# Optimization experiments

Hardware: AMD Instinct MI355X
Metric: run time of the kernel (lower is better)

The kernel has to match this reference:

```python
import jax, jax.numpy as jnp
import numpy as np
from jax import lax


def _lstm_encode(x_seq, W_ih, W_hh, b_ih, b_hh):
    """Run a single-layer LSTM over x_seq (B,S,F); return final (h, c), each (B,H).
    PyTorch gate order: i, f, g, o."""
    B = x_seq.shape[0]
    H = W_hh.shape[1]
    # Precompute input projections for the whole sequence: (B,S,4H)
    xg = jnp.einsum('bsf,gf->bsg', x_seq, W_ih) + b_ih + b_hh

    def step(carry, xg_t):
        h, c = carry
        gates = xg_t + h @ W_hh.T  # (B,4H)
        i, f, g, o = jnp.split(gates, 4, axis=-1)
        c = jax.nn.sigmoid(f) * c + jax.nn.sigmoid(i) * jnp.tanh(g)
        h = jax.nn.sigmoid(o) * jnp.tanh(c)
        return (h, c), None

    h0 = jnp.zeros((B, H), dtype=x_seq.dtype)
    c0 = jnp.zeros((B, H), dtype=x_seq.dtype)
    (h, c), _ = lax.scan(step, (h0, c0), jnp.swapaxes(xg, 0, 1))
    return h, c


def setup_inputs() -> dict:
    key = jax.random.key(0)
    ks = jax.random.split(key, 8)
    B, S, F, H, T = 256, 512, 64, 1024, 64
    s_in = 1.0 / np.sqrt(F)
    s_h = 1.0 / np.sqrt(H)
    return {
        'input_sequence': jax.random.normal(ks[0], (B, S, F), dtype=jnp.float32),
        'W_ih_enc': jax.random.normal(ks[1], (4 * H, F), dtype=jnp.float32) * s_in,
        'W_hh_enc': jax.random.normal(ks[2], (4 * H, H), dtype=jnp.float32) * s_h,
        'b_ih_enc': jnp.zeros((4 * H,), dtype=jnp.float32),
        'b_hh_enc': jnp.zeros((4 * H,), dtype=jnp.float32),
        'W_ih_dec': jax.random.normal(ks[3], (4 * H, F), dtype=jnp.float32) * s_in,
        'W_hh_dec': jax.random.normal(ks[4], (4 * H, H), dtype=jnp.float32) * s_h,
        'b_ih_dec': jnp.zeros((4 * H,), dtype=jnp.float32),
        'b_hh_dec': jnp.zeros((4 * H,), dtype=jnp.float32),
        'W_fc': jax.random.normal(ks[5], (F, H), dtype=jnp.float32) * s_h,
        'b_fc': jnp.zeros((F,), dtype=jnp.float32),
        'prediction_length': T,
    }


def reference(input_sequence, W_ih_enc, W_hh_enc, b_ih_enc, b_hh_enc,
              W_ih_dec, W_hh_dec, b_ih_dec, b_hh_dec, W_fc, b_fc,
              prediction_length):
    # Encoder: summarize past sequence into final (h, c)
    h, c = _lstm_encode(input_sequence, W_ih_enc, W_hh_enc, b_ih_enc, b_hh_enc)

    b_dec = b_ih_dec + b_hh_dec
    x0 = input_sequence[:, -1, :]  # (B,F) last observed step

    def dec_step(carry, _):
        h, c, x = carry
        gates = x @ W_ih_dec.T + h @ W_hh_dec.T + b_dec  # (B,4H)
        i, f, g, o = jnp.split(gates, 4, axis=-1)
        c = jax.nn.sigmoid(f) * c + jax.nn.sigmoid(i) * jnp.tanh(g)
        h = jax.nn.sigmoid(o) * jnp.tanh(c)
        pred = h @ W_fc.T + b_fc  # (B,F)
        return (h, c, pred), pred

    _, preds = lax.scan(dec_step, (h, c, x0), None, length=prediction_length)
    # preds: (T,B,F) -> (B,T,F)
    return jnp.swapaxes(preds, 0, 1)
```

## Files before the change

### kernel.cpp

```cpp
#include <hip/hip_runtime.h>
#include <hip/hip_cooperative_groups.h>
#include <stdint.h>
#include <stddef.h>

namespace cg = cooperative_groups;


typedef short s16x8 __attribute__((ext_vector_type(8)));
typedef float f32x4 __attribute__((ext_vector_type(4)));
typedef float f32x16 __attribute__((ext_vector_type(16)));

#define LDS_BYTES  156416
#define RED_OFF    139264
#define BIASG_OFF  155904
#define BIASFC_OFF 156160

#define WS_FLAGS 0
#define WS_HRING 12288
#define WS_WFC   4206592

#define HBUF_ELEMS 262144
#define GO_BASE    2304

__device__ __forceinline__ unsigned short f2bf(float f) {
  union { unsigned int i; float f; } v;
  v.f = f;
  unsigned int i = v.i;
  return (unsigned short)((i + 0x7FFFu + ((i >> 16) & 1u)) >> 16);
}
__device__ __forceinline__ float sigm(float x) { return 1.f / (1.f + __expf(-x)); }
__device__ __forceinline__ float tanh_f(float x) {
  float e = __expf(2.f * x);
  return 1.f - 2.f / (e + 1.f);
}

__device__ __forceinline__ void load_wg(unsigned short* wl, float* biasg,
    const float* Wih, const float* Whh, const float* bih, const float* bhh,
    int n, int wave, int lane, int tid) {
  const int l31 = lane & 31;
  const int kh8 = (lane >> 5) << 3;
  for (int f = wave; f < 136; f += 8) {
    const int s  = f >> 1;
    const int t2 = f & 1;
    const int col = t2 * 32 + l31;
    const int k0  = s * 16 + kh8;
    const int r   = (col >> 4) * 1024 + n * 16 + (col & 15);
    const float* src = (s < 4) ? (Wih + (size_t)r * 64 + k0)
                               : (Whh + (size_t)r * 1024 + (k0 - 64));
    s16x8 w;
#pragma unroll
    for (int j = 0; j < 8; ++j) ((unsigned short*)&w)[j] = f2bf(src[j]);
    *(s16x8*)(wl + (size_t)f * 512 + lane * 8) = w;
  }
  if (tid < 64) {
    const int r = (tid >> 4) * 1024 + n * 16 + (tid & 15);
    biasg[tid] = bih[r] + bhh[r];
  }
}

__device__ __forceinline__ void red_write32(float* red, const f32x16 (&acc)[2],
                                            int lane, int mh, const float* bias) {
#pragma unroll
  for (int t2 = 0; t2 < 2; ++t2)
#pragma unroll
    for (int r = 0; r < 16; ++r) {
      const int row = mh * 32 + (r & 3) + ((r >> 2) << 3) + ((lane >> 5) << 2);
      const int col = t2 * 32 + (lane & 31);
      float v = acc[t2][r];
      if (bias) v += bias[col];
      red[row * 65 + col] = v;
    }
}
__device__ __forceinline__ void red_add32(float* red, const f32x16 (&acc)[2],
                                          int lane, int mh) {
#pragma unroll
  for (int t2 = 0; t2 < 2; ++t2)
#pragma unroll
    for (int r = 0; r < 16; ++r) {
      const int row = mh * 32 + (r & 3) + ((r >> 2) << 3) + ((lane >> 5) << 2);
      const int col = t2 * 32 + (lane & 31);
      atomicAdd(red + row * 65 + col, acc[t2][r]);
    }
}

__global__ void __launch_bounds__(512, 1) seq2seq_lstm(
    const float* __restrict__ xin,
    const float* __restrict__ Wih_e,
    const float* __restrict__ Whh_e,
    const float* __restrict__ bih_e,
    const float* __restrict__ bhh_e,
    const float* __restrict__ Wih_d,
    const float* __restrict__ Whh_d,
    const float* __restrict__ bih_d,
    const float* __restrict__ bhh_d,
    const float* __restrict__ Wfc,
    const float* __restrict__ bfc,
    float* __restrict__ out,
    unsigned short* __restrict__ hring,
    unsigned short* __restrict__ wfcb,
    unsigned int* __restrict__ flags) {
  extern __shared__ char smem[];
  unsigned short* wl = (unsigned short*)smem;
  float* red    = (float*)(smem + RED_OFF);
  float* biasg  = (float*)(smem + BIASG_OFF);
  float* biasfc = (float*)(smem + BIASFC_OFF);

  cg::grid_group grid = cg::this_grid();

  const int tid  = threadIdx.x;
  const int wave = tid >> 6;
  const int lane = tid & 63;
  const int wg   = blockIdx.x;
  const int m    = wg & 3;
  const int n    = wg >> 2;
  const int bm   = m << 6;
  const int l31  = lane & 31;
  const int kh8  = (lane >> 5) << 3;
  const int mh   = wave & 1;
  const int q    = wave >> 1;
  const int ks0  = q * 17;
  const int mrow = bm + mh * 32 + l31;
  const int ar   = tid >> 2;
  const int auu  = (tid & 3) << 2;

  load_wg(wl, biasg, Wih_e, Whh_e, bih_e, bhh_e, n, wave, lane, tid);

  {
    if (tid < 256) {
      unsigned short* hinit = hring + (size_t)7 * HBUF_ELEMS;
      const size_t hq = ((size_t)n * 4096 + (size_t)(bm + ar) * 16 + auu) >> 2;
      __hip_atomic_store((unsigned long long*)hinit + hq, 0ull,
                         __ATOMIC_RELAXED, __HIP_MEMORY_SCOPE_AGENT);
      wfcb[wg * 256 + tid] = f2bf(Wfc[wg * 256 + tid]);
    }
    if (tid < 9)
      __hip_atomic_store(flags + wg * 9 + tid, 0u,
                         __ATOMIC_RELAXED, __HIP_MEMORY_SCOPE_AGENT);
    if (wg == 0 && tid < 16)
      __hip_atomic_store(flags + GO_BASE + tid * 32, 0u,
                         __ATOMIC_RELAXED, __HIP_MEMORY_SCOPE_AGENT);
  }
  __syncthreads();
  grid.sync();

  float cst[4] = {0.f, 0.f, 0.f, 0.f};

  for (int gs = 0; gs < 576; ++gs) {
    const bool dec = (gs >= 512);
    const int t = gs - 512;

    if ((gs & 7) == 0 && gs != 0) {
      if (tid == 0) __builtin_amdgcn_fence(__ATOMIC_ACQUIRE, "agent");
      __syncthreads();
    }

    if (gs == 512) {
      __syncthreads();
      load_wg(wl, biasg, Wih_d, Whh_d, bih_d, bhh_d, n, wave, lane, tid);
      if (tid < 64) biasfc[tid] = bfc[tid];
      __syncthreads();
    }
    const unsigned short* hb = hring + (size_t)((gs + 7) & 7) * HBUF_ELEMS;
    unsigned short* hnx      = hring + (size_t)(gs & 7) * HBUF_ELEMS;

    s16x8 areg[17];
#pragma unroll
    for (int i = 0; i < 17; ++i) {
      const int s = ks0 + i;
      if (s < 4) {
        const int fk = s * 16 + kh8;
        if (!dec || t == 0) {
          const int tt = dec ? 511 : gs;
          const float* p = xin + (size_t)mrow * 32768 + tt * 64 + fk;
          s16x8 av;
#pragma unroll
          for (int j = 0; j < 8; ++j) ((unsigned short*)&av)[j] = f2bf(p[j]);
          areg[i] = av;
        } else {
          s16x8 av;
#pragma unroll
          for (int j = 0; j < 8; ++j)
            ((unsigned short*)&av)[j] = f2bf(red[(mh * 32 + l31) * 65 + fk + j]);
          areg[i] = av;
        }
      } else {
        areg[i] = *(const s16x8*)(hb + (size_t)(s - 4) * 4096 +
                                  (size_t)mrow * 16 + kh8);
      }
    }

    f32x16 acc[2] = {};
#pragma unroll
    for (int i = 0; i < 17; ++i) {
      const int s = ks0 + i;
      const s16x8 b0 = *(const s16x8*)(wl + (size_t)(s * 2 + 0) * 512 + lane * 8);
      const s16x8 b1 = *(const s16x8*)(wl + (size_t)(s * 2 + 1) * 512 + lane * 8);
      acc[0] = __builtin_amdgcn_mfma_f32_32x32x16_bf16(areg[i], b0, acc[0], 0, 0, 0);
      acc[1] = __builtin_amdgcn_mfma_f32_32x32x16_bf16(areg[i], b1, acc[1], 0, 0, 0);
    }

    if (q == 0) red_write32(red, acc, lane, mh, nullptr);
    __syncthreads();
    if (q != 0) red_add32(red, acc, lane, mh);
    __syncthreads();

    if (tid < 256) {
      float hn[4];
#pragma unroll
      for (int j = 0; j < 4; ++j) {
        const int u = auu + j;
        const float gi = red[ar * 65 + u]      + biasg[u];
        const float gf = red[ar * 65 + 16 + u] + biasg[16 + u];
        const float gg = red[ar * 65 + 32 + u] + biasg[32 + u];
        const float go = red[ar * 65 + 48 + u] + biasg[48 + u];
        const float c = sigm(gf) * cst[j] + sigm(gi) * tanh_f(gg);
        cst[j] = c;
        hn[j] = sigm(go) * tanh_f(c);
      }
      union { unsigned short u[4]; unsigned long long ull; } pk;
#pragma unroll
      for (int j = 0; j < 4; ++j) pk.u[j] = f2bf(hn[j]);
      const size_t hq = ((size_t)n * 4096 + (size_t)(bm + ar) * 16 + auu) >> 2;
      __hip_atomic_store((unsigned long long*)hnx + hq, pk.ull,
                         __ATOMIC_RELAXED, __HIP_MEMORY_SCOPE_AGENT);
    }
    __syncthreads();

    if (tid == 0) {
      unsigned int* fl = flags + m * 576 + gs;
      unsigned int old = __hip_atomic_fetch_add(fl, 1u, __ATOMIC_RELAXED,
                                                __HIP_MEMORY_SCOPE_AGENT);
      if (old == 63u) {
        const unsigned int stamp = (unsigned int)gs + 1u;
#pragma unroll
        for (int sb = 0; sb < 4; ++sb)
          __hip_atomic_store(flags + GO_BASE + (m * 4 + sb) * 32, stamp,
                             __ATOMIC_RELAXED, __HIP_MEMORY_SCOPE_AGENT);
      } else {
        unsigned int* go = flags + GO_BASE + (m * 4 + (n >> 4)) * 32;
        for (;;) {
          unsigned int v = __hip_atomic_fetch_add(go, 0u, __ATOMIC_RELAXED,
                                                  __HIP_MEMORY_SCOPE_AGENT);
          if (v > (unsigned int)gs) break;
        }
      }
      if (dec) __builtin_amdgcn_fence(__ATOMIC_ACQUIRE, "agent");
    }
    __syncthreads();

    if (dec && (n == 0 || t < 63)) {
      f32x16 pacc[2] = {};
      const int ps0 = q * 16;
#pragma unroll 4
      for (int i = 0; i < 16; ++i) {
        const int k = (ps0 + i) * 16 + kh8;
        const unsigned short* hp =
            hnx + (size_t)(ps0 + i) * 4096 + (size_t)mrow * 16 + kh8;
        const unsigned short* wp = wfcb + (size_t)l31 * 1024 + k;
        const s16x8 a0 = *(const s16x8*)hp;
        const s16x8 b0 = *(const s16x8*)wp;
        const s16x8 b1 = *(const s16x8*)(wp + 32 * 1024);
        pacc[0] = __builtin_amdgcn_mfma_f32_32x32x16_bf16(a0, b0, pacc[0], 0, 0, 0);
        pacc[1] = __builtin_amdgcn_mfma_f32_32x32x16_bf16(a0, b1, pacc[1], 0, 0, 0);
      }
      if (q == 0) red_write32(red, pacc, lane, mh, biasfc);
      __syncthreads();
      if (q != 0) red_add32(red, pacc, lane, mh);
      __syncthreads();
      if (n == 0) {
        const int ob = tid >> 3;
        const int oc = (tid & 7) << 3;
        float* op = out + (size_t)(bm + ob) * 4096 + t * 64 + oc;
#pragma unroll
        for (int jj = 0; jj < 8; jj += 4) {
          f32x4 v = { red[ob * 65 + oc + jj],     red[ob * 65 + oc + jj + 1],
                      red[ob * 65 + oc + jj + 2], red[ob * 65 + oc + jj + 3] };
          *(f32x4*)(op + jj) = v;
        }
      }
      __syncthreads();
    }
  }
}

extern "C" void kernel_launch(void* const* d_in, const int* in_sizes, int n_in,
                              void* d_out, int out_size, void* d_ws, size_t ws_size,
                              hipStream_t stream) {
  (void)in_sizes; (void)n_in; (void)out_size; (void)ws_size;
  const float* xin   = (const float*)d_in[0];
  const float* Wih_e = (const float*)d_in[1];
  const float* Whh_e = (const float*)d_in[2];
  const float* bih_e = (const float*)d_in[3];
  const float* bhh_e = (const float*)d_in[4];
  const float* Wih_d = (const float*)d_in[5];
  const float* Whh_d = (const float*)d_in[6];
  const float* bih_d = (const float*)d_in[7];
  const float* bhh_d = (const float*)d_in[8];
  const float* Wfc   = (const float*)d_in[9];
  const float* bfc   = (const float*)d_in[10];
  float* out = (float*)d_out;

  char* ws = (char*)d_ws;
  unsigned int* flags   = (unsigned int*)(ws + WS_FLAGS);
  unsigned short* hring = (unsigned short*)(ws + WS_HRING);
  unsigned short* wfcb  = (unsigned short*)(ws + WS_WFC);

  hipFuncSetAttribute((const void*)seq2seq_lstm,
                      hipFuncAttributeMaxDynamicSharedMemorySize, LDS_BYTES);

  void* args[] = {
    (void*)&xin, (void*)&Wih_e, (void*)&Whh_e, (void*)&bih_e, (void*)&bhh_e,
    (void*)&Wih_d, (void*)&Whh_d, (void*)&bih_d, (void*)&bhh_d,
    (void*)&Wfc, (void*)&bfc, (void*)&out, (void*)&hring,
    (void*)&wfcb, (void*)&flags
  };
  hipLaunchCooperativeKernel((const void*)seq2seq_lstm, dim3(256), dim3(512),
                             args, LDS_BYTES, stream);
}
```

Before: 14.46 ms.

## Replace per-row barrier counter with per-producer flag slots and fine-grained waits

```diff
diff --git a/kernel.cpp b/kernel.cpp
--- a/kernel.cpp
+++ b/kernel.cpp
@@ -20,7 +20,15 @@
 #define WS_WFC   4206592
 
 #define HBUF_ELEMS 262144
-#define GO_BASE    2304
+
+#define SLOT(mm,nn) (((mm) * 64 + ((((nn) & 15) << 2) | ((nn) >> 4))) * 8)
+
+__device__ __forceinline__ void sleep_bk(int bk) {
+  if (bk == 0)      __builtin_amdgcn_s_sleep(1);
+  else if (bk == 1) __builtin_amdgcn_s_sleep(2);
+  else if (bk == 2) __builtin_amdgcn_s_sleep(4);
+  else              __builtin_amdgcn_s_sleep(8);
+}
 
 __device__ __forceinline__ unsigned short f2bf(float f) {
   union { unsigned int i; float f; } v;
@@ -133,11 +141,8 @@
                          __ATOMIC_RELAXED, __HIP_MEMORY_SCOPE_AGENT);
       wfcb[wg * 256 + tid] = f2bf(Wfc[wg * 256 + tid]);
     }
-    if (tid < 9)
-      __hip_atomic_store(flags + wg * 9 + tid, 0u,
-                         __ATOMIC_RELAXED, __HIP_MEMORY_SCOPE_AGENT);
-    if (wg == 0 && tid < 16)
-      __hip_atomic_store(flags + GO_BASE + tid * 32, 0u,
+    if (tid == 0)
+      __hip_atomic_store(flags + SLOT(m, n), 0u,
                          __ATOMIC_RELAXED, __HIP_MEMORY_SCOPE_AGENT);
   }
   __syncthreads();
@@ -162,6 +167,23 @@
     }
     const unsigned short* hb = hring + (size_t)((gs + 7) & 7) * HBUF_ELEMS;
     unsigned short* hnx      = hring + (size_t)(gs & 7) * HBUF_ELEMS;
+
+    {
+      const int s = ks0 + lane;
+      const bool need = (lane < 17) && (s >= 4);
+      unsigned int* sp = flags + (need ? SLOT(m, s - 4) : SLOT(m, 0));
+      const unsigned int thr = (unsigned int)gs;
+      int bk = 0;
+      for (;;) {
+        unsigned int v = need ? __hip_atomic_fetch_add(sp, 0u, __ATOMIC_RELAXED,
+                                                       __HIP_MEMORY_SCOPE_AGENT)
+                              : thr;
+        if (__all((int)(v >= thr))) break;
+        sleep_bk(bk);
+        if (bk < 3) ++bk;
+      }
+      __builtin_amdgcn_fence(__ATOMIC_ACQUIRE, "workgroup");
+    }
 
     s16x8 areg[17];
 #pragma unroll
@@ -226,29 +248,30 @@
     }
     __syncthreads();
 
-    if (tid == 0) {
-      unsigned int* fl = flags + m * 576 + gs;
-      unsigned int old = __hip_atomic_fetch_add(fl, 1u, __ATOMIC_RELAXED,
-                                                __HIP_MEMORY_SCOPE_AGENT);
-      if (old == 63u) {
-        const unsigned int stamp = (unsigned int)gs + 1u;
-#pragma unroll
-        for (int sb = 0; sb < 4; ++sb)
-          __hip_atomic_store(flags + GO_BASE + (m * 4 + sb) * 32, stamp,
-                             __ATOMIC_RELAXED, __HIP_MEMORY_SCOPE_AGENT);
-      } else {
-        unsigned int* go = flags + GO_BASE + (m * 4 + (n >> 4)) * 32;
+    if (tid == 0)
+      __hip_atomic_store(flags + SLOT(m, n), (unsigned int)gs + 1u,
+                         __ATOMIC_RELAXED, __HIP_MEMORY_SCOPE_AGENT);
+
+    if (dec && (n == 0 || t < 63)) {
+      {
+        const bool need = (lane < 16);
+        const int sl = q * 16 + (lane & 15);
+        unsigned int* sp = flags + SLOT(m, sl);
+        const unsigned int thr = (unsigned int)gs + 1u;
+        int bk = 0;
         for (;;) {
-          unsigned int v = __hip_atomic_fetch_add(go, 0u, __ATOMIC_RELAXED,
-                                                  __HIP_MEMORY_SCOPE_AGENT);
-          if (v > (unsigned int)gs) break;
+          unsigned int v = need ? __hip_atomic_fetch_add(sp, 0u, __ATOMIC_RELAXED,
+                                                         __HIP_MEMORY_SCOPE_AGENT)
+                                : thr;
+          if (__all((int)(v >= thr))) break;
+          sleep_bk(bk);
+          if (bk < 3) ++bk;
         }
       }
-      if (dec) __builtin_amdgcn_fence(__ATOMIC_ACQUIRE, "agent");
-    }
-    __syncthreads();
-
-    if (dec && (n == 0 || t < 63)) {
+      __syncthreads();
+      if (tid == 0) __builtin_amdgcn_fence(__ATOMIC_ACQUIRE, "agent");
+      __syncthreads();
+
       f32x16 pacc[2] = {};
       const int ps0 = q * 16;
 #pragma unroll 4
```

Result: no change. 14.23 ms (-1.6%).
